# Performance work log

Measured on AMD Instinct MI355X. Metric: run time of the kernel, lower is better.

Reference implementation:

```python
import jax, jax.numpy as jnp
import numpy as np

OUT = 7  # STN crop size hard-coded as (7, 7) in the original build()


def gather_pairs(num_points):
    # replicates the pred_gather_indexes construction in build()
    pairs = [[0, 0]]
    si = 1
    while si + 2 < num_points:
        pairs.append([si, si])
        pairs.append([si + 1, si + 2])
        si += 3
    pairs.append([si, si])
    pairs.append([si + 1, si + 1])
    return np.asarray(pairs, dtype=np.int32)


def _sample_one(feat, theta):
    # feat [H,W,C], theta [6] = affine row-major 2x3; classic STN bilinear crop
    H, W, _ = feat.shape
    lin = jnp.linspace(-1.0, 1.0, OUT)
    gy, gx = jnp.meshgrid(lin, lin, indexing='ij')
    xs = theta[0] * gx + theta[1] * gy + theta[2]
    ys = theta[3] * gx + theta[4] * gy + theta[5]
    px = (xs + 1.0) * (W - 1) * 0.5
    py = (ys + 1.0) * (H - 1) * 0.5
    x0 = jnp.floor(px)
    y0 = jnp.floor(py)
    wx = px - x0
    wy = py - y0
    x0i = jnp.clip(x0, 0, W - 1).astype(jnp.int32)
    x1i = jnp.clip(x0 + 1, 0, W - 1).astype(jnp.int32)
    y0i = jnp.clip(y0, 0, H - 1).astype(jnp.int32)
    y1i = jnp.clip(y0 + 1, 0, H - 1).astype(jnp.int32)
    Ia = feat[y0i, x0i]
    Ib = feat[y1i, x0i]
    Ic = feat[y0i, x1i]
    Id = feat[y1i, x1i]
    wa = ((1 - wx) * (1 - wy))[..., None]
    wb = ((1 - wx) * wy)[..., None]
    wc = (wx * (1 - wy))[..., None]
    wd = (wx * wy)[..., None]
    return wa * Ia + wb * Ib + wc * Ic + wd * Id  # [OUT,OUT,C]

# vmap over boxes then over batch -> feat [B,H,W,C], theta [B,n,6] -> [B,n,7,7,C]
_sample = jax.vmap(jax.vmap(_sample_one, in_axes=(None, 0)), in_axes=(0, 0))


def _hierarchy(pred_prev, feat, W1, b1, W2, b2, W3, b3):
    B = pred_prev.shape[0]
    centers = (pred_prev[:, :-1] + pred_prev[:, 1:]) * 0.5
    diffs = (pred_prev[:, 1:] - pred_prev[:, :-1]) * 0.5
    cx, cy = centers[..., 0], centers[..., 1]
    dx, dy = diffs[..., 0], diffs[..., 1]
    # fixed (non-trainable) dense with constant kernel -> theta = [dx,-dy,-cx,dy,dx,-cy]
    theta = jnp.stack([dx, -dy, -cx, dy, dx, -cy], axis=-1)  # [B,n,6]
    theta = jax.lax.stop_gradient(theta)  # stop_gradient=True default
    rois = _sample(feat, theta)  # [B,n,7,7,C]
    n = theta.shape[1]
    x = rois.reshape(B * n, -1)
    f1 = jnp.tanh(x @ W1 + b1)
    f2 = jnp.tanh(f1 @ W2 + b2)
    f3 = f2 @ W3 + b3 + jnp.asarray([-1.0, 0.0, 0.0, 0.0, 1.0, 0.0], dtype=f2.dtype)
    npnt = n * 3
    pts = f3.reshape(B, npnt, 2)
    # fixed homography dense: (x,y) -> (x,y,-1)
    hom = jnp.concatenate([pts, -jnp.ones((B, npnt, 1), dtype=pts.dtype)], axis=-1)
    theta_e = jnp.repeat(theta, 3, axis=1).reshape(B, npnt, 2, 3)
    pt = jnp.einsum('bpij,bpj->bpi', theta_e, hom)  # [B,npnt,2]
    idx = gather_pairs(npnt)  # [m,2]
    pg = pt[:, idx]  # [B,m,2,2]
    return pg.mean(axis=2)  # [B,m,2]


def setup_inputs() -> dict:
    key = jax.random.key(0)
    ks = jax.random.split(key, 16)
    B = 32
    d = {
        'last_feature': jax.random.normal(ks[0], (B, 4096), jnp.float32),
        'conv4_3': jax.random.normal(ks[1], (B, 28, 28, 512), jnp.float32),
        'conv3_3': jax.random.normal(ks[2], (B, 56, 56, 256), jnp.float32),
        'conv2_2': jax.random.normal(ks[3], (B, 112, 112, 128), jnp.float32),
        'W_trans': jax.random.normal(ks[4], (4096, 18), jnp.float32) * 0.005,
        'b_trans': jnp.zeros((18,), jnp.float32),
    }
    C = [512, 256, 128]
    for h in range(3):
        kk = jax.random.split(ks[5 + h], 3)
        fan = OUT * OUT * C[h]
        d[f'W1_{h}'] = jax.random.normal(kk[0], (fan, 1024), jnp.float32) * 0.001
        d[f'b1_{h}'] = jnp.zeros((1024,), jnp.float32)
        d[f'W2_{h}'] = jax.random.normal(kk[1], (1024, 256), jnp.float32) * 0.02
        d[f'b2_{h}'] = jnp.zeros((256,), jnp.float32)
        d[f'W3_{h}'] = jax.random.normal(kk[2], (256, 6), jnp.float32) * 0.01
        d[f'b3_{h}'] = jnp.zeros((6,), jnp.float32)
    return d


def reference(last_feature, conv4_3, conv3_3, conv2_2, W_trans, b_trans,
              W1_0, b1_0, W2_0, b2_0, W3_0, b3_0,
              W1_1, b1_1, W2_1, b2_1, W3_1, b3_1,
              W1_2, b1_2, W2_2, b2_2, W3_2, b3_2):
    B = last_feature.shape[0]
    pred = (last_feature @ W_trans + b_trans).reshape(B, 9, 2)
    feats = [conv4_3, conv3_3, conv2_2]
    heads = [(W1_0, b1_0, W2_0, b2_0, W3_0, b3_0),
             (W1_1, b1_1, W2_1, b2_1, W3_1, b3_1),
             (W1_2, b1_2, W2_2, b2_2, W3_2, b3_2)]
    for h in range(3):
        pred = _hierarchy(pred, feats[h], *heads[h])
    return pred[:, :-1, :] * 6.0  # [B,64,2]
```

## Files before the change

kernel.cpp:

```cpp
#include <hip/hip_runtime.h>
#include <hip/hip_bf16.h>
#include <math.h>

typedef __attribute__((ext_vector_type(8))) short   short8;
typedef __attribute__((ext_vector_type(4))) float   floatx4;

#define OFF_PRED_A   0ULL
#define OFF_PRED_B   16384ULL
#define OFF_PT       32768ULL
#define OFF_W2T      65536ULL
#define OFF_F1       2097152ULL
#define OFF_P2       4194304ULL
#define OFF_X        8388608ULL
#define OFF_P1       21233664ULL
#define OFF_W1T      38010880ULL

__global__ __launch_bounds__(64) void pred_init_kernel(
    const float* __restrict__ lf, const float* __restrict__ Wt,
    const float* __restrict__ bt, float* __restrict__ pred)
{
    int blk = blockIdx.x;
    int j = blk % 18, b = blk / 18;
    int lane = threadIdx.x;
    const float* lfb = lf + (size_t)b * 4096;
    float acc = 0.f;
    for (int k = lane; k < 4096; k += 64)
        acc += lfb[k] * Wt[(size_t)k * 18 + j];
    #pragma unroll
    for (int off = 32; off >= 1; off >>= 1)
        acc += __shfl_xor(acc, off, 64);
    if (lane == 0) pred[b * 18 + j] = acc + bt[j];
}

__global__ __launch_bounds__(256) void transpose_cvt(
    const float* __restrict__ src, __hip_bfloat16* __restrict__ dst, int R, int C)
{
    __shared__ float tile[32][33];
    int tx = threadIdx.x & 31, ty = threadIdx.x >> 5;
    int bx = blockIdx.x, by = blockIdx.y;
    #pragma unroll
    for (int k = 0; k < 4; ++k) {
        int r = by * 32 + ty + k * 8, c = bx * 32 + tx;
        tile[ty + k * 8][tx] = (r < R && c < C) ? src[(size_t)r * C + c] : 0.f;
    }
    __syncthreads();
    #pragma unroll
    for (int k = 0; k < 4; ++k) {
        int r = bx * 32 + ty + k * 8;
        int c = by * 32 + tx;
        if (r < C && c < R)
            dst[(size_t)r * R + c] = __float2bfloat16(tile[tx][ty + k * 8]);
    }
}

__global__ __launch_bounds__(256) void sample_kernel(
    const float* __restrict__ feat, int H, int W, int lc,
    const float* __restrict__ predPrev, int nseg,
    __hip_bfloat16* __restrict__ x)
{
    int blk = blockIdx.x;
    int i = blk % nseg, b = blk / nseg;
    const float* pp = predPrev + (size_t)(b * (nseg + 1) + i) * 2;
    float x0 = pp[0], y0 = pp[1], x1 = pp[2], y1 = pp[3];
    float cx = 0.5f * (x0 + x1), cy = 0.5f * (y0 + y1);
    float dx = 0.5f * (x1 - x0), dy = 0.5f * (y1 - y0);
    int C = 1 << lc;
    int total = 49 << lc;
    size_t rowbase = (size_t)blk * total;
    const float* fb = feat + (size_t)b * H * W * C;
    for (int j = threadIdx.x; j < total; j += 256) {
        int pix = j >> lc;
        int c = j & (C - 1);
        int oy = pix / 7, ox = pix - oy * 7;
        float gx = (float)(ox - 3) * (1.f / 3.f);
        float gy = (float)(oy - 3) * (1.f / 3.f);
        float xs = dx * gx - dy * gy - cx;
        float ys = dy * gx + dx * gy - cy;
        float px = (xs + 1.f) * (float)(W - 1) * 0.5f;
        float py = (ys + 1.f) * (float)(H - 1) * 0.5f;
        float x0f = floorf(px), y0f = floorf(py);
        float wx = px - x0f, wy = py - y0f;
        int xi0 = (int)fminf(fmaxf(x0f,       0.f), (float)(W - 1));
        int xi1 = (int)fminf(fmaxf(x0f + 1.f, 0.f), (float)(W - 1));
        int yi0 = (int)fminf(fmaxf(y0f,       0.f), (float)(H - 1));
        int yi1 = (int)fminf(fmaxf(y0f + 1.f, 0.f), (float)(H - 1));
        float Ia = fb[((size_t)yi0 * W + xi0) * C + c];
        float Ib = fb[((size_t)yi1 * W + xi0) * C + c];
        float Ic = fb[((size_t)yi0 * W + xi1) * C + c];
        float Id = fb[((size_t)yi1 * W + xi1) * C + c];
        float va = (1.f - wx) * (1.f - wy) * Ia + (1.f - wx) * wy * Ib
                 + wx * (1.f - wy) * Ic + wx * wy * Id;
        x[rowbase + j] = __float2bfloat16(va);
    }
}

__global__ __launch_bounds__(64) void gemm_mfma(
    const __hip_bfloat16* __restrict__ A, const __hip_bfloat16* __restrict__ Bt,
    float* __restrict__ P, int M, int N, int K, int slice)
{
    int lane = threadIdx.x;
    int lo = lane & 15, hi = lane >> 4;
    int mt = blockIdx.x, nt = blockIdx.y, s = blockIdx.z;
    const short* Ap = (const short*)A + (size_t)(mt * 64 + lo) * K + (size_t)s * slice + hi * 8;
    const short* Bp = (const short*)Bt + (size_t)(nt * 64 + lo) * K + (size_t)s * slice + hi * 8;

    floatx4 acc[4][4];
    #pragma unroll
    for (int a = 0; a < 4; ++a)
        #pragma unroll
        for (int b = 0; b < 4; ++b)
            acc[a][b] = floatx4{0.f, 0.f, 0.f, 0.f};

    short8 ca[4], cb[4], na[4], nb[4];
    int nch = slice >> 5;

#define LDF(da, db, koff)                                                     \
    {                                                                         \
        _Pragma("unroll")                                                     \
        for (int q = 0; q < 4; ++q)                                           \
            da[q] = *(const short8*)(Ap + (size_t)q * 16 * K + (koff));       \
        _Pragma("unroll")                                                     \
        for (int q = 0; q < 4; ++q)                                           \
            db[q] = *(const short8*)(Bp + (size_t)q * 16 * K + (koff));       \
    }
#define MM(da, db)                                                            \
    {                                                                         \
        _Pragma("unroll")                                                     \
        for (int mi = 0; mi < 4; ++mi)                                        \
            _Pragma("unroll")                                                 \
            for (int ni = 0; ni < 4; ++ni)                                    \
                acc[mi][ni] = __builtin_amdgcn_mfma_f32_16x16x32_bf16(        \
                    da[mi], db[ni], acc[mi][ni], 0, 0, 0);                    \
    }

    LDF(ca, cb, 0)
    for (int c = 0; c + 1 < nch; c += 2) {
        LDF(na, nb, (c + 1) * 32)
        MM(ca, cb)
        if (c + 2 < nch) LDF(ca, cb, (c + 2) * 32)
        MM(na, nb)
    }
    if (nch & 1) MM(ca, cb)

    #pragma unroll
    for (int mi = 0; mi < 4; ++mi) {
        int row0 = mt * 64 + mi * 16 + hi * 4;
        #pragma unroll
        for (int ni = 0; ni < 4; ++ni) {
            int col = nt * 64 + ni * 16 + lo;
            #pragma unroll
            for (int r = 0; r < 4; ++r)
                P[((size_t)s * M + row0 + r) * N + col] = acc[mi][ni][r];
        }
    }
#undef LDF
#undef MM
}

__global__ __launch_bounds__(256) void reduce_tanh_kernel(
    const float* __restrict__ P1, const float* __restrict__ b1,
    __hip_bfloat16* __restrict__ f1, int M, int S)
{
    int e = blockIdx.x * 256 + threadIdx.x;
    int n = e & 1023;
    float v = b1[n];
    size_t stride = (size_t)M * 1024;
    for (int s = 0; s < S; ++s) v += P1[(size_t)s * stride + e];
    f1[e] = __float2bfloat16(tanhf(v));
}

__global__ __launch_bounds__(64) void gemm3pts_kernel(
    const float* __restrict__ P2, const float* __restrict__ b2,
    const float* __restrict__ W3, const float* __restrict__ b3,
    const float* __restrict__ predPrev, float* __restrict__ pt,
    int nseg, int lns, int M)
{
    int m = blockIdx.x;
    int lane = threadIdx.x;
    float acc[6] = {0.f, 0.f, 0.f, 0.f, 0.f, 0.f};
    #pragma unroll
    for (int q = 0; q < 4; ++q) {
        int k = lane + q * 64;
        float v = b2[k];
        #pragma unroll
        for (int s = 0; s < 4; ++s)
            v += P2[((size_t)s * M + m) * 256 + k];
        v = tanhf(v);
        const float* w = W3 + (size_t)k * 6;
        #pragma unroll
        for (int j = 0; j < 6; ++j) acc[j] += v * w[j];
    }
    #pragma unroll
    for (int j = 0; j < 6; ++j)
        #pragma unroll
        for (int off = 32; off >= 1; off >>= 1)
            acc[j] += __shfl_xor(acc[j], off, 64);
    if (lane == 0) {
        int i = m & (nseg - 1);
        int b = m >> lns;
        const float* pp = predPrev + (size_t)(b * (nseg + 1) + i) * 2;
        float x0 = pp[0], y0 = pp[1], x1 = pp[2], y1 = pp[3];
        float cx = 0.5f * (x0 + x1), cy = 0.5f * (y0 + y1);
        float dx = 0.5f * (x1 - x0), dy = 0.5f * (y1 - y0);
        float f[6];
        #pragma unroll
        for (int j = 0; j < 6; ++j) f[j] = acc[j] + b3[j];
        f[0] -= 1.f;
        f[4] += 1.f;
        int npnt = nseg * 3;
        size_t base = ((size_t)b * npnt + 3 * i) * 2;
        #pragma unroll
        for (int s = 0; s < 3; ++s) {
            float px = f[2 * s], py = f[2 * s + 1];
            pt[base + 2 * s]     = dx * px - dy * py + cx;
            pt[base + 2 * s + 1] = dy * px + dx * py + cy;
        }
    }
}

__global__ __launch_bounds__(256) void pairs_kernel(
    const float* __restrict__ pt, float* __restrict__ outp, int nseg, int last)
{
    int npnt = nseg * 3;
    int Pn = 2 * nseg + 1;
    int idx = blockIdx.x * 256 + threadIdx.x;
    int total = 32 * Pn * 2;
    if (idx >= total) return;
    int c = idx & 1;
    int t = idx >> 1;
    int p = t % Pn, b = t / Pn;
    int i1, i2;
    if (p == 0) { i1 = i2 = 0; }
    else if (p >= Pn - 2) { i1 = i2 = npnt - (Pn - p); }
    else {
        int q = (p - 1) >> 1, r = (p - 1) & 1;
        int si = 1 + 3 * q;
        if (r == 0) { i1 = i2 = si; }
        else        { i1 = si + 1; i2 = si + 2; }
    }
    float v = 0.5f * (pt[((size_t)b * npnt + i1) * 2 + c] +
                      pt[((size_t)b * npnt + i2) * 2 + c]);
    if (last) {
        if (p < Pn - 1) outp[((size_t)b * (Pn - 1) + p) * 2 + c] = 6.f * v;
    } else {
        outp[((size_t)b * Pn + p) * 2 + c] = v;
    }
}

extern "C" void kernel_launch(void* const* d_in, const int* in_sizes, int n_in,
                              void* d_out, int out_size, void* d_ws, size_t ws_size,
                              hipStream_t stream) {
    (void)in_sizes; (void)n_in; (void)out_size; (void)ws_size;
    const float* lf  = (const float*)d_in[0];
    const float* feats[3] = {(const float*)d_in[1], (const float*)d_in[2], (const float*)d_in[3]};
    const float* Wtr = (const float*)d_in[4];
    const float* btr = (const float*)d_in[5];

    char* ws = (char*)d_ws;
    float* predA = (float*)(ws + OFF_PRED_A);
    float* predB = (float*)(ws + OFF_PRED_B);
    float* ptbuf = (float*)(ws + OFF_PT);
    __hip_bfloat16* f1  = (__hip_bfloat16*)(ws + OFF_F1);
    float* P2           = (float*)(ws + OFF_P2);
    __hip_bfloat16* xb  = (__hip_bfloat16*)(ws + OFF_X);
    float* P1           = (float*)(ws + OFF_P1);
    __hip_bfloat16* W1T = (__hip_bfloat16*)(ws + OFF_W1T);

    pred_init_kernel<<<dim3(32 * 18), 64, 0, stream>>>(lf, Wtr, btr, predA);

    for (int h = 0; h < 3; ++h) {
        __hip_bfloat16* w2t = (__hip_bfloat16*)(ws + OFF_W2T + (size_t)h * 524288);
        transpose_cvt<<<dim3(256 / 32, 1024 / 32), 256, 0, stream>>>(
            (const float*)d_in[8 + 6 * h], w2t, 1024, 256);
    }

    const int Hs[3]   = {28, 56, 112};
    const int lcs[3]  = {9, 8, 7};
    const int nsegs[3] = {8, 16, 32};
    const int lnss[3]  = {3, 4, 5};
    const int Ks[3]   = {25088, 12544, 6272};
    const int S1s[3]  = {16, 8, 4};

    float* predPrev = predA;
    float* predNext = predB;
    for (int h = 0; h < 3; ++h) {
        int H = Hs[h], W = Hs[h], lc = lcs[h];
        int nseg = nsegs[h], M = 32 * nseg, K = Ks[h], S1 = S1s[h];
        const float* W1 = (const float*)d_in[6 + 6 * h];
        const float* b1 = (const float*)d_in[7 + 6 * h];
        const float* b2 = (const float*)d_in[9 + 6 * h];
        const float* W3 = (const float*)d_in[10 + 6 * h];
        const float* b3 = (const float*)d_in[11 + 6 * h];
        __hip_bfloat16* w2t = (__hip_bfloat16*)(ws + OFF_W2T + (size_t)h * 524288);

        transpose_cvt<<<dim3(1024 / 32, K / 32), 256, 0, stream>>>(W1, W1T, K, 1024);

        sample_kernel<<<dim3(32 * nseg), 256, 0, stream>>>(
            feats[h], H, W, lc, predPrev, nseg, xb);

        gemm_mfma<<<dim3(M / 64, 1024 / 64, S1), 64, 0, stream>>>(
            xb, W1T, P1, M, 1024, K, K / S1);

        reduce_tanh_kernel<<<dim3(M * 1024 / 256), 256, 0, stream>>>(P1, b1, f1, M, S1);

        gemm_mfma<<<dim3(M / 64, 256 / 64, 4), 64, 0, stream>>>(
            f1, w2t, P2, M, 256, 1024, 256);

        gemm3pts_kernel<<<dim3(M), 64, 0, stream>>>(
            P2, b2, W3, b3, predPrev, ptbuf, nseg, lnss[h], M);

        int Pn = 2 * nseg + 1;
        int last = (h == 2);
        float* dst = last ? (float*)d_out : predNext;
        pairs_kernel<<<dim3((32 * Pn * 2 + 255) / 256), 256, 0, stream>>>(
            ptbuf, dst, nseg, last);

        float* tmp = predPrev; predPrev = predNext; predNext = tmp;
    }
}
```

Baseline: 843.5 us.

## Fuse setup transposes, vectorize sampling, fold pairs into consumers, widen GEMM blocks

All W1/W2 transpose-to-bf16 conversions and the initial prediction GEMV are merged into one large setup kernel, replacing about seven separate launches. The STN sampler now computes bilinear offsets and weights once per output pixel in shared memory and uses float4 loads and packed bf16 stores. The per-level pairs kernel is removed: sample and gemm3pts rebuild box endpoints directly from the previous level's points, and only one final pairs kernel remains. GEMMs now run four waves per block covering four N tiles, with more K splits (28/14/7 for layer 1, 8 for layer 2), which adds partial-sum traffic for the reductions to read.

```diff
diff --git a/kernel.cpp b/kernel.cpp
--- a/kernel.cpp
+++ b/kernel.cpp
@@ -5,102 +5,159 @@
 typedef __attribute__((ext_vector_type(8))) short   short8;
 typedef __attribute__((ext_vector_type(4))) float   floatx4;
 
-#define OFF_PRED_A   0ULL
-#define OFF_PRED_B   16384ULL
-#define OFF_PT       32768ULL
-#define OFF_W2T      65536ULL
+#define OFF_PRED     0ULL
+#define OFF_PTA      16384ULL
+#define OFF_PTB      65536ULL
+#define OFF_W2T      131072ULL
 #define OFF_F1       2097152ULL
 #define OFF_P2       4194304ULL
-#define OFF_X        8388608ULL
-#define OFF_P1       21233664ULL
-#define OFF_W1T      38010880ULL
-
-__global__ __launch_bounds__(64) void pred_init_kernel(
-    const float* __restrict__ lf, const float* __restrict__ Wt,
-    const float* __restrict__ bt, float* __restrict__ pred)
-{
+#define OFF_X        16777216ULL
+#define OFF_P1       33554432ULL
+#define OFF_W1T      67108864ULL
+
+__device__ inline void pair_idx(int p, int Pn, int npnt, int& i1, int& i2) {
+    if (p == 0) { i1 = i2 = 0; }
+    else if (p >= Pn - 2) { i1 = i2 = npnt - (Pn - p); }
+    else {
+        int q = (p - 1) >> 1, r = (p - 1) & 1;
+        int si = 1 + 3 * q;
+        if (r == 0) { i1 = i2 = si; } else { i1 = si + 1; i2 = si + 2; }
+    }
+}
+__device__ inline float2 pred_point(const float* pred0, const float* pt,
+                                    int nsegP, int b, int p) {
+    if (nsegP == 0) {
+        const float* q = pred0 + ((size_t)b * 9 + p) * 2;
+        return float2{q[0], q[1]};
+    }
+    int npnt = nsegP * 3, Pn = 2 * nsegP + 1;
+    int i1, i2; pair_idx(p, Pn, npnt, i1, i2);
+    const float* a = pt + ((size_t)b * npnt + i1) * 2;
+    const float* c = pt + ((size_t)b * npnt + i2) * 2;
+    return float2{0.5f * (a[0] + c[0]), 0.5f * (a[1] + c[1])};
+}
+
+struct SetupArgs {
+    const float* W1s[3]; __hip_bfloat16* W1T[3]; int K[3];
+    const float* W2s[3]; __hip_bfloat16* W2T[3];
+    const float* lf; const float* Wt; const float* bt; float* pred;
+};
+
+__device__ inline void transpose_tile(const float* __restrict__ src,
+                                      __hip_bfloat16* __restrict__ dst,
+                                      int R, int C, int rowT, int colT,
+                                      float (*tile)[33]) {
+    int tx = threadIdx.x & 31, ty = threadIdx.x >> 5;
+    int r0 = rowT * 32, c0 = colT * 32;
+    #pragma unroll
+    for (int k = 0; k < 4; ++k)
+        tile[ty + k * 8][tx] = src[(size_t)(r0 + ty + k * 8) * C + c0 + tx];
+    __syncthreads();
+    #pragma unroll
+    for (int k = 0; k < 4; ++k)
+        dst[(size_t)(c0 + ty + k * 8) * R + r0 + tx] =
+            __float2bfloat16(tile[tx][ty + k * 8]);
+}
+
+__global__ __launch_bounds__(256) void setup_kernel(SetupArgs a) {
+    __shared__ float tile[32][33];
+    int id = blockIdx.x;
+    if (id < 43904) {
+        int h = (id < 25088) ? 0 : (id < 37632 ? 1 : 2);
+        int base = (h == 0) ? 0 : (h == 1 ? 25088 : 37632);
+        int l = id - base;
+        transpose_tile(a.W1s[h], a.W1T[h], a.K[h], 1024, l >> 5, l & 31, tile);
+    } else if (id < 44672) {
+        int l = id - 43904;
+        int h = l >> 8; int t = l & 255;
+        transpose_tile(a.W2s[h], a.W2T[h], 1024, 256, t >> 3, t & 7, tile);
+    } else {
+        int l = id - 44672;
+        int wave = threadIdx.x >> 6, lane = threadIdx.x & 63;
+        int task = l * 4 + wave;
+        int j = task % 18, b = task / 18;
+        const float* lfb = a.lf + (size_t)b * 4096;
+        float acc = 0.f;
+        for (int k = lane; k < 4096; k += 64)
+            acc += lfb[k] * a.Wt[(size_t)k * 18 + j];
+        #pragma unroll
+        for (int off = 32; off >= 1; off >>= 1)
+            acc += __shfl_xor(acc, off, 64);
+        if (lane == 0) a.pred[b * 18 + j] = acc + a.bt[j];
+    }
+}
+
+__global__ __launch_bounds__(256) void sample_kernel(
+    const float* __restrict__ feat, int Wd, int lc,
+    const float* __restrict__ pred0, const float* __restrict__ ptPrev, int nsegP,
+    int lns, __hip_bfloat16* __restrict__ x)
+{
+    int nseg = 1 << lns;
     int blk = blockIdx.x;
-    int j = blk % 18, b = blk / 18;
-    int lane = threadIdx.x;
-    const float* lfb = lf + (size_t)b * 4096;
-    float acc = 0.f;
-    for (int k = lane; k < 4096; k += 64)
-        acc += lfb[k] * Wt[(size_t)k * 18 + j];
-    #pragma unroll
-    for (int off = 32; off >= 1; off >>= 1)
-        acc += __shfl_xor(acc, off, 64);
-    if (lane == 0) pred[b * 18 + j] = acc + bt[j];
-}
-
-__global__ __launch_bounds__(256) void transpose_cvt(
-    const float* __restrict__ src, __hip_bfloat16* __restrict__ dst, int R, int C)
-{
-    __shared__ float tile[32][33];
-    int tx = threadIdx.x & 31, ty = threadIdx.x >> 5;
-    int bx = blockIdx.x, by = blockIdx.y;
-    #pragma unroll
-    for (int k = 0; k < 4; ++k) {
-        int r = by * 32 + ty + k * 8, c = bx * 32 + tx;
-        tile[ty + k * 8][tx] = (r < R && c < C) ? src[(size_t)r * C + c] : 0.f;
-    }
-    __syncthreads();
-    #pragma unroll
-    for (int k = 0; k < 4; ++k) {
-        int r = bx * 32 + ty + k * 8;
-        int c = by * 32 + tx;
-        if (r < C && c < R)
-            dst[(size_t)r * R + c] = __float2bfloat16(tile[tx][ty + k * 8]);
-    }
-}
-
-__global__ __launch_bounds__(256) void sample_kernel(
-    const float* __restrict__ feat, int H, int W, int lc,
-    const float* __restrict__ predPrev, int nseg,
-    __hip_bfloat16* __restrict__ x)
-{
-    int blk = blockIdx.x;
-    int i = blk % nseg, b = blk / nseg;
-    const float* pp = predPrev + (size_t)(b * (nseg + 1) + i) * 2;
-    float x0 = pp[0], y0 = pp[1], x1 = pp[2], y1 = pp[3];
-    float cx = 0.5f * (x0 + x1), cy = 0.5f * (y0 + y1);
-    float dx = 0.5f * (x1 - x0), dy = 0.5f * (y1 - y0);
+    int i = blk & (nseg - 1), b = blk >> lns;
+    float2 p0 = pred_point(pred0, ptPrev, nsegP, b, i);
+    float2 p1 = pred_point(pred0, ptPrev, nsegP, b, i + 1);
+    float cx = 0.5f * (p0.x + p1.x), cy = 0.5f * (p0.y + p1.y);
+    float dx = 0.5f * (p1.x - p0.x), dy = 0.5f * (p1.y - p0.y);
+
+    __shared__ float4 wv[49];
+    __shared__ int4   ov[49];
+    int t = threadIdx.x;
     int C = 1 << lc;
-    int total = 49 << lc;
-    size_t rowbase = (size_t)blk * total;
-    const float* fb = feat + (size_t)b * H * W * C;
-    for (int j = threadIdx.x; j < total; j += 256) {
-        int pix = j >> lc;
-        int c = j & (C - 1);
-        int oy = pix / 7, ox = pix - oy * 7;
+    if (t < 49) {
+        int oy = t / 7, ox = t - oy * 7;
         float gx = (float)(ox - 3) * (1.f / 3.f);
         float gy = (float)(oy - 3) * (1.f / 3.f);
         float xs = dx * gx - dy * gy - cx;
         float ys = dy * gx + dx * gy - cy;
-        float px = (xs + 1.f) * (float)(W - 1) * 0.5f;
-        float py = (ys + 1.f) * (float)(H - 1) * 0.5f;
+        float fW = (float)(Wd - 1);
+        float px = (xs + 1.f) * fW * 0.5f;
+        float py = (ys + 1.f) * fW * 0.5f;
         float x0f = floorf(px), y0f = floorf(py);
         float wx = px - x0f, wy = py - y0f;
-        int xi0 = (int)fminf(fmaxf(x0f,       0.f), (float)(W - 1));
-        int xi1 = (int)fminf(fmaxf(x0f + 1.f, 0.f), (float)(W - 1));
-        int yi0 = (int)fminf(fmaxf(y0f,       0.f), (float)(H - 1));
-        int yi1 = (int)fminf(fmaxf(y0f + 1.f, 0.f), (float)(H - 1));
-        float Ia = fb[((size_t)yi0 * W + xi0) * C + c];
-        float Ib = fb[((size_t)yi1 * W + xi0) * C + c];
-        float Ic = fb[((size_t)yi0 * W + xi1) * C + c];
-        float Id = fb[((size_t)yi1 * W + xi1) * C + c];
-        float va = (1.f - wx) * (1.f - wy) * Ia + (1.f - wx) * wy * Ib
-                 + wx * (1.f - wy) * Ic + wx * wy * Id;
-        x[rowbase + j] = __float2bfloat16(va);
-    }
-}
-
-__global__ __launch_bounds__(64) void gemm_mfma(
+        int xi0 = (int)fminf(fmaxf(x0f,       0.f), fW);
+        int xi1 = (int)fminf(fmaxf(x0f + 1.f, 0.f), fW);
+        int yi0 = (int)fminf(fmaxf(y0f,       0.f), fW);
+        int yi1 = (int)fminf(fmaxf(y0f + 1.f, 0.f), fW);
+        int c4 = C >> 2;
+        ov[t] = int4{(yi0 * Wd + xi0) * c4, (yi1 * Wd + xi0) * c4,
+                     (yi0 * Wd + xi1) * c4, (yi1 * Wd + xi1) * c4};
+        wv[t] = float4{(1.f - wx) * (1.f - wy), (1.f - wx) * wy,
+                       wx * (1.f - wy),         wx * wy};
+    }
+    __syncthreads();
+
+    const float4* fb4 = (const float4*)(feat + (size_t)b * Wd * Wd * C);
+    int c4 = 1 << (lc - 2);
+    int total4 = 49 << (lc - 2);
+    size_t rowbase = (size_t)blk * (49 << lc);
+    for (int j = t; j < total4; j += 256) {
+        int pix = j >> (lc - 2);
+        int cc  = j & (c4 - 1);
+        int4 o = ov[pix]; float4 w = wv[pix];
+        float4 Ia = fb4[o.x + cc], Ib = fb4[o.y + cc];
+        float4 Ic = fb4[o.z + cc], Id = fb4[o.w + cc];
+        float4 v;
+        v.x = w.x * Ia.x + w.y * Ib.x + w.z * Ic.x + w.w * Id.x;
+        v.y = w.x * Ia.y + w.y * Ib.y + w.z * Ic.y + w.w * Id.y;
+        v.z = w.x * Ia.z + w.y * Ib.z + w.z * Ic.z + w.w * Id.z;
+        v.w = w.x * Ia.w + w.y * Ib.w + w.z * Ic.w + w.w * Id.w;
+        __hip_bfloat16 h0 = __float2bfloat16(v.x), h1 = __float2bfloat16(v.y);
+        __hip_bfloat16 h2 = __float2bfloat16(v.z), h3 = __float2bfloat16(v.w);
+        ushort4 u = {*(unsigned short*)&h0, *(unsigned short*)&h1,
+                     *(unsigned short*)&h2, *(unsigned short*)&h3};
+        *(ushort4*)(x + rowbase + ((size_t)pix << lc) + cc * 4) = u;
+    }
+}
+
+__global__ __launch_bounds__(256) void gemm_mfma4(
     const __hip_bfloat16* __restrict__ A, const __hip_bfloat16* __restrict__ Bt,
     float* __restrict__ P, int M, int N, int K, int slice)
 {
-    int lane = threadIdx.x;
+    int lane = threadIdx.x & 63;
+    int wave = threadIdx.x >> 6;
     int lo = lane & 15, hi = lane >> 4;
-    int mt = blockIdx.x, nt = blockIdx.y, s = blockIdx.z;
+    int mt = blockIdx.x, nt = blockIdx.y * 4 + wave, s = blockIdx.z;
     const short* Ap = (const short*)A + (size_t)(mt * 64 + lo) * K + (size_t)s * slice + hi * 8;
     const short* Bp = (const short*)Bt + (size_t)(nt * 64 + lo) * K + (size_t)s * slice + hi * 8;
 
@@ -172,18 +229,19 @@
 __global__ __launch_bounds__(64) void gemm3pts_kernel(
     const float* __restrict__ P2, const float* __restrict__ b2,
     const float* __restrict__ W3, const float* __restrict__ b3,
-    const float* __restrict__ predPrev, float* __restrict__ pt,
-    int nseg, int lns, int M)
+    const float* __restrict__ pred0, const float* __restrict__ ptPrev, int nsegP,
+    float* __restrict__ pt, int lns, int M)
 {
     int m = blockIdx.x;
     int lane = threadIdx.x;
+    int nseg = 1 << lns;
     float acc[6] = {0.f, 0.f, 0.f, 0.f, 0.f, 0.f};
     #pragma unroll
     for (int q = 0; q < 4; ++q) {
         int k = lane + q * 64;
         float v = b2[k];
         #pragma unroll
-        for (int s = 0; s < 4; ++s)
+        for (int s = 0; s < 8; ++s)
             v += P2[((size_t)s * M + m) * 256 + k];
         v = tanhf(v);
         const float* w = W3 + (size_t)k * 6;
@@ -198,10 +256,10 @@
     if (lane == 0) {
         int i = m & (nseg - 1);
         int b = m >> lns;
-        const float* pp = predPrev + (size_t)(b * (nseg + 1) + i) * 2;
-        float x0 = pp[0], y0 = pp[1], x1 = pp[2], y1 = pp[3];
-        float cx = 0.5f * (x0 + x1), cy = 0.5f * (y0 + y1);
-        float dx = 0.5f * (x1 - x0), dy = 0.5f * (y1 - y0);
+        float2 p0 = pred_point(pred0, ptPrev, nsegP, b, i);
+        float2 p1 = pred_point(pred0, ptPrev, nsegP, b, i + 1);
+        float cx = 0.5f * (p0.x + p1.x), cy = 0.5f * (p0.y + p1.y);
+        float dx = 0.5f * (p1.x - p0.x), dy = 0.5f * (p1.y - p0.y);
         float f[6];
         #pragma unroll
         for (int j = 0; j < 6; ++j) f[j] = acc[j] + b3[j];
@@ -218,103 +276,90 @@
     }
 }
 
-__global__ __launch_bounds__(256) void pairs_kernel(
-    const float* __restrict__ pt, float* __restrict__ outp, int nseg, int last)
-{
-    int npnt = nseg * 3;
-    int Pn = 2 * nseg + 1;
+__global__ __launch_bounds__(256) void pairs_final_kernel(
+    const float* __restrict__ pt, float* __restrict__ outp, int nsegP)
+{
+    int npnt = nsegP * 3;
+    int Pn = 2 * nsegP + 1;
     int idx = blockIdx.x * 256 + threadIdx.x;
     int total = 32 * Pn * 2;
     if (idx >= total) return;
     int c = idx & 1;
     int t = idx >> 1;
     int p = t % Pn, b = t / Pn;
-    int i1, i2;
-    if (p == 0) { i1 = i2 = 0; }
-    else if (p >= Pn - 2) { i1 = i2 = npnt - (Pn - p); }
-    else {
-        int q = (p - 1) >> 1, r = (p - 1) & 1;
-        int si = 1 + 3 * q;
-        if (r == 0) { i1 = i2 = si; }
-        else        { i1 = si + 1; i2 = si + 2; }
-    }
+    int i1, i2; pair_idx(p, Pn, npnt, i1, i2);
     float v = 0.5f * (pt[((size_t)b * npnt + i1) * 2 + c] +
                       pt[((size_t)b * npnt + i2) * 2 + c]);
-    if (last) {
-        if (p < Pn - 1) outp[((size_t)b * (Pn - 1) + p) * 2 + c] = 6.f * v;
-    } else {
-        outp[((size_t)b * Pn + p) * 2 + c] = v;
-    }
+    if (p < Pn - 1) outp[((size_t)b * (Pn - 1) + p) * 2 + c] = 6.f * v;
 }
 
 extern "C" void kernel_launch(void* const* d_in, const int* in_sizes, int n_in,
                               void* d_out, int out_size, void* d_ws, size_t ws_size,
                               hipStream_t stream) {
     (void)in_sizes; (void)n_in; (void)out_size; (void)ws_size;
-    const float* lf  = (const float*)d_in[0];
     const float* feats[3] = {(const float*)d_in[1], (const float*)d_in[2], (const float*)d_in[3]};
-    const float* Wtr = (const float*)d_in[4];
-    const float* btr = (const float*)d_in[5];
 
     char* ws = (char*)d_ws;
-    float* predA = (float*)(ws + OFF_PRED_A);
-    float* predB = (float*)(ws + OFF_PRED_B);
-    float* ptbuf = (float*)(ws + OFF_PT);
-    __hip_bfloat16* f1  = (__hip_bfloat16*)(ws + OFF_F1);
-    float* P2           = (float*)(ws + OFF_P2);
-    __hip_bfloat16* xb  = (__hip_bfloat16*)(ws + OFF_X);
-    float* P1           = (float*)(ws + OFF_P1);
-    __hip_bfloat16* W1T = (__hip_bfloat16*)(ws + OFF_W1T);
-
-    pred_init_kernel<<<dim3(32 * 18), 64, 0, stream>>>(lf, Wtr, btr, predA);
-
+    float* predA = (float*)(ws + OFF_PRED);
+    float* ptA   = (float*)(ws + OFF_PTA);
+    float* ptB   = (float*)(ws + OFF_PTB);
+    __hip_bfloat16* f1 = (__hip_bfloat16*)(ws + OFF_F1);
+    float* P2          = (float*)(ws + OFF_P2);
+    __hip_bfloat16* xb = (__hip_bfloat16*)(ws + OFF_X);
+    float* P1          = (float*)(ws + OFF_P1);
+
+    const int Ks[3]  = {25088, 12544, 6272};
+    const int S1s[3] = {28, 14, 7};
+    const int lcs[3] = {9, 8, 7};
+    const int Hs[3]  = {28, 56, 112};
+    const int lnss[3] = {3, 4, 5};
+
+    SetupArgs sa;
+    size_t w1off = 0;
     for (int h = 0; h < 3; ++h) {
-        __hip_bfloat16* w2t = (__hip_bfloat16*)(ws + OFF_W2T + (size_t)h * 524288);
-        transpose_cvt<<<dim3(256 / 32, 1024 / 32), 256, 0, stream>>>(
-            (const float*)d_in[8 + 6 * h], w2t, 1024, 256);
-    }
-
-    const int Hs[3]   = {28, 56, 112};
-    const int lcs[3]  = {9, 8, 7};
-    const int nsegs[3] = {8, 16, 32};
-    const int lnss[3]  = {3, 4, 5};
-    const int Ks[3]   = {25088, 12544, 6272};
-    const int S1s[3]  = {16, 8, 4};
-
-    float* predPrev = predA;
-    float* predNext = predB;
+        sa.W1s[h] = (const float*)d_in[6 + 6 * h];
+        sa.W1T[h] = (__hip_bfloat16*)(ws + OFF_W1T + w1off);
+        sa.K[h]   = Ks[h];
+        w1off += (size_t)Ks[h] * 1024 * 2;
+        sa.W2s[h] = (const float*)d_in[8 + 6 * h];
+        sa.W2T[h] = (__hip_bfloat16*)(ws + OFF_W2T + (size_t)h * 524288);
+    }
+    sa.lf = (const float*)d_in[0];
+    sa.Wt = (const float*)d_in[4];
+    sa.bt = (const float*)d_in[5];
+    sa.pred = predA;
+
+    setup_kernel<<<dim3(44816), 256, 0, stream>>>(sa);
+
+    float* pts[2] = {ptA, ptB};
+    const float* ptPrev = nullptr;
+    int nsegP = 0;
     for (int h = 0; h < 3; ++h) {
-        int H = Hs[h], W = Hs[h], lc = lcs[h];
-        int nseg = nsegs[h], M = 32 * nseg, K = Ks[h], S1 = S1s[h];
-        const float* W1 = (const float*)d_in[6 + 6 * h];
+        int lns = lnss[h], nseg = 1 << lns, M = 32 * nseg;
+        int K = Ks[h], S1 = S1s[h];
         const float* b1 = (const float*)d_in[7 + 6 * h];
         const float* b2 = (const float*)d_in[9 + 6 * h];
         const float* W3 = (const float*)d_in[10 + 6 * h];
         const float* b3 = (const float*)d_in[11 + 6 * h];
-        __hip_bfloat16* w2t = (__hip_bfloat16*)(ws + OFF_W2T + (size_t)h * 524288);
-
-        transpose_cvt<<<dim3(1024 / 32, K / 32), 256, 0, stream>>>(W1, W1T, K, 1024);
 
         sample_kernel<<<dim3(32 * nseg), 256, 0, stream>>>(
-            feats[h], H, W, lc, predPrev, nseg, xb);
-
-        gemm_mfma<<<dim3(M / 64, 1024 / 64, S1), 64, 0, stream>>>(
-            xb, W1T, P1, M, 1024, K, K / S1);
+            feats[h], Hs[h], lcs[h], predA, ptPrev, nsegP, lns, xb);
+
+        gemm_mfma4<<<dim3(M / 64, 4, S1), 256, 0, stream>>>(
+            xb, sa.W1T[h], P1, M, 1024, K, K / S1);
 
         reduce_tanh_kernel<<<dim3(M * 1024 / 256), 256, 0, stream>>>(P1, b1, f1, M, S1);
 
-        gemm_mfma<<<dim3(M / 64, 256 / 64, 4), 64, 0, stream>>>(
-            f1, w2t, P2, M, 256, 1024, 256);
-
+        gemm_mfma4<<<dim3(M / 64, 1, 8), 256, 0, stream>>>(
+            f1, sa.W2T[h], P2, M, 256, 1024, 128);
+
+        float* ptCur = pts[h & 1];
         gemm3pts_kernel<<<dim3(M), 64, 0, stream>>>(
-            P2, b2, W3, b3, predPrev, ptbuf, nseg, lnss[h], M);
-
-        int Pn = 2 * nseg + 1;
-        int last = (h == 2);
-        float* dst = last ? (float*)d_out : predNext;
-        pairs_kernel<<<dim3((32 * Pn * 2 + 255) / 256), 256, 0, stream>>>(
-            ptbuf, dst, nseg, last);
-
-        float* tmp = predPrev; predPrev = predNext; predNext = tmp;
-    }
-}
+            P2, b2, W3, b3, predA, ptPrev, nsegP, ptCur, lns, M);
+
+        ptPrev = ptCur; nsegP = nseg;
+    }
+
+    pairs_final_kernel<<<dim3((32 * 65 * 2 + 255) / 256), 256, 0, stream>>>(
+        ptA, (float*)d_out, 32);
+}
```

Result: faster. 773.7 us (-8.3%).
